# Optimization experiments

Measured on AMD Instinct MI355X. Metric: run time of the kernel, lower is better.

The kernel has to match this reference:

```python
import jax, jax.numpy as jnp
import numpy as np

T = 512        # num tokens
H = 2048       # hidden_size
I = 1024       # moe_intermediate_size
E = 32         # n_routed_experts
K = 8          # num_experts_per_tok
NG = 8         # n_group
TG = 4         # topk_group
NSH = 2        # n_shared_experts
SCALE = 2.5    # routed_scaling_factor


def setup_inputs() -> dict:
    key = jax.random.key(0)
    ks = jax.random.split(key, 7)
    s = 0.02  # weight init scale
    return {
        "hidden_states": jax.random.normal(ks[0], (T, H), jnp.float32),
        "gate_w": jax.random.normal(ks[1], (E, H), jnp.float32) * s,
        "gate_bias": jax.random.normal(ks[2], (E,), jnp.float32) * s,
        "w_gate_up": jax.random.normal(ks[3], (E, H, 2 * I), jnp.float32) * s,
        "w_down": jax.random.normal(ks[4], (E, I, H), jnp.float32) * s,
        "shared_w_gate_up": jax.random.normal(ks[5], (H, 2 * NSH * I), jnp.float32) * s,
        "shared_w_down": jax.random.normal(ks[6], (NSH * I, H), jnp.float32) * s,
    }


def _grouped_topk(logits, bias):
    # DeepSeek-V3 noaux_tc routing with sigmoid scoring.
    t = logits.shape[0]
    s = jax.nn.sigmoid(logits)                       # [T,E] routing weights source
    sc = s + bias[None, :]                           # scores used for selection only
    grp = sc.reshape(t, NG, E // NG)
    # group score = sum of top-2 expert scores in each group
    gscore = jax.lax.top_k(grp, 2)[0].sum(-1)        # [T,NG]
    _, gidx = jax.lax.top_k(gscore, TG)              # [T,TG]
    gmask = jnp.zeros((t, NG), bool).at[jnp.arange(t)[:, None], gidx].set(True)
    emask = jnp.repeat(gmask, E // NG, axis=1)       # [T,E]
    masked = jnp.where(emask, sc, -jnp.inf)
    _, ids = jax.lax.top_k(masked, K)                # [T,K] expert ids
    w = jnp.take_along_axis(s, ids, axis=1)          # weights from un-biased scores
    w = w / jnp.sum(w, -1, keepdims=True)            # renormalize
    return w * SCALE, ids


def reference(hidden_states, gate_w, gate_bias, w_gate_up, w_down,
              shared_w_gate_up, shared_w_down):
    x = hidden_states                                 # [T,H]
    logits = x @ gate_w.T                             # [T,E] (gate in fp32)
    w, ids = _grouped_topk(logits, gate_bias)
    t = x.shape[0]
    # scatter top-k weights into dense combine matrix [T,E]
    cw = jnp.zeros((t, E), x.dtype).at[jnp.arange(t)[:, None], ids].add(w)
    # routed experts: silu-gated MLP per expert, combined by routing weights
    gu = jnp.einsum('th,ehi->tei', x, w_gate_up)      # [T,E,2I]
    gate, up = jnp.split(gu, 2, axis=-1)
    act = jax.nn.silu(gate) * up                      # SiluAndMul, [T,E,I]
    act = act * cw[:, :, None]                        # apply combine weight pre-down
    routed = jnp.einsum('tei,eih->th', act, w_down)   # [T,H]
    # shared experts MLP
    sgu = x @ shared_w_gate_up
    sg, su = jnp.split(sgu, 2, axis=-1)
    shared = (jax.nn.silu(sg) * su) @ shared_w_down   # [T,H]
    return routed + shared
```

## Files before the change

### kernel.cpp

```cpp
#include <hip/hip_runtime.h>
#include <hip/hip_bf16.h>

#define T_TOK 512
#define HD    2048
#define ID    1024
#define NE    32
#define TOPK  8
#define NGRP  8
#define TGRP  4
#define NSH   2
#define SCALE 2.5f
#define NEXP  (NE + NSH)
#define KT1   64
#define KT2   32

typedef __attribute__((ext_vector_type(8))) short bf16x8;
typedef __attribute__((ext_vector_type(4))) float f32x4;
typedef unsigned short u16;
typedef unsigned long long u64;
typedef unsigned int u32;

__device__ __forceinline__ u16 f2bf(float f) {
    union { float f; u32 u; } a; a.f = f;
    u32 r = a.u + 0x7FFFu + ((a.u >> 16) & 1u);
    return (u16)(r >> 16);
}

__device__ __forceinline__ u32 pk2(float lo, float hi) {
    union { float f; u32 u; } a, b; a.f = lo; b.f = hi;
    u32 rl = a.u + 0x7FFFu + ((a.u >> 16) & 1u);
    u32 rh = b.u + 0x7FFFu + ((b.u >> 16) & 1u);
    return (rh & 0xFFFF0000u) | (rl >> 16);
}

__device__ __forceinline__ f32x4 mfma16(bf16x8 a, bf16x8 b, f32x4 c) {
    return __builtin_amdgcn_mfma_f32_16x16x32_bf16(a, b, c, 0, 0, 0);
}

union Q { uint4 q; bf16x8 v; };

__device__ __forceinline__ void glds16(const void* g, void* l) {
    __builtin_amdgcn_global_load_lds(
        (const __attribute__((address_space(1))) u32*)g,
        (__attribute__((address_space(3))) u32*)l, 16, 0, 0);
}

__device__ __forceinline__ bf16x8 bfrag(const float* Bt, int c, int g) {
    const int clo = c ^ (g << 4);
    const float* p_lo = Bt + g * 512 + clo;
    const float* p_hi = Bt + g * 512 + 2048 + (clo ^ 64);
    union { u32 d[4]; bf16x8 v; } r;
    r.d[0] = pk2(p_lo[0],   p_lo[128]);
    r.d[1] = pk2(p_lo[256], p_lo[384]);
    r.d[2] = pk2(p_hi[0],   p_hi[128]);
    r.d[3] = pk2(p_hi[256], p_hi[384]);
    return r.v;
}

__global__ __launch_bounds__(256) void k_xconv(const float* __restrict__ x,
                                               u16* __restrict__ xb) {
    int gt = blockIdx.x * 256 + threadIdx.x;
    const float* s = x + (size_t)(gt >> 6) * HD + (gt & 63) * 32;
    float v[32];
#pragma unroll
    for (int i = 0; i < 8; i++) {
        float4 f = *(const float4*)(s + i * 4);
        v[i*4] = f.x; v[i*4+1] = f.y; v[i*4+2] = f.z; v[i*4+3] = f.w;
    }
    union { u16 o[32]; uint4 q[4]; } pk;
#pragma unroll
    for (int g = 0; g < 4; g++)
#pragma unroll
        for (int jj = 0; jj < 8; jj++) {
            int r = (jj < 4) ? 4*g + jj : 4*g + 16 + (jj - 4);
            pk.o[g*8 + jj] = f2bf(v[r]);
        }
    uint4* d = (uint4*)(xb + (size_t)gt * 32);
#pragma unroll
    for (int i = 0; i < 4; i++) d[i] = pk.q[i];
}

__global__ __launch_bounds__(64) void k_route(const float* __restrict__ x,
                                              const float* __restrict__ gw,
                                              const float* __restrict__ gb,
                                              int* __restrict__ counts,
                                              int* __restrict__ tok_ids,
                                              float* __restrict__ tok_w,
                                              int* __restrict__ slotmap) {
    const int t = blockIdx.x, lane = threadIdx.x;
    __shared__ float xr[HD];
    __shared__ float slog[NE], ss[NE], scb[NE], smm[NE];
    for (int i = lane; i < HD; i += 64) xr[i] = x[(size_t)t * HD + i];
    __syncthreads();
    const int e = lane >> 1, half = lane & 1;
    const float4* w4 = (const float4*)(gw + (size_t)e * HD + half * 1024);
    const float4* x4 = (const float4*)(xr + half * 1024);
    float acc = 0.f;
#pragma unroll 8
    for (int i = 0; i < 256; i++) {
        float4 a = x4[i], b = w4[i];
        acc += a.x * b.x + a.y * b.y + a.z * b.z + a.w * b.w;
    }
    acc += __shfl_xor(acc, 1, 64);
    if (!half) slog[e] = acc;
    __syncthreads();
    if (lane == 0) {
        for (int i = 0; i < NE; i++) {
            float s = 1.f / (1.f + __expf(-slog[i]));
            ss[i] = s; scb[i] = s + gb[i];
        }
        float gsc[NGRP];
        for (int g = 0; g < NGRP; g++) {
            float a = scb[4*g], b = scb[4*g+1], c = scb[4*g+2], d = scb[4*g+3];
            float mab = fmaxf(a,b), nab = fminf(a,b), mcd = fmaxf(c,d), ncd = fminf(c,d);
            float m2 = (mab >= mcd) ? fmaxf(nab, mcd) : fmaxf(ncd, mab);
            gsc[g] = fmaxf(mab, mcd) + m2;
        }
        int gmask = 0;
        for (int it = 0; it < TGRP; it++) {
            float best = -1e30f; int bi = 0;
            for (int g = 0; g < NGRP; g++)
                if (!((gmask >> g) & 1) && gsc[g] > best) { best = gsc[g]; bi = g; }
            gmask |= 1 << bi;
        }
        for (int i = 0; i < NE; i++)
            smm[i] = ((gmask >> (i >> 2)) & 1) ? scb[i] : -1e30f;
        int ids[TOPK]; float wv[TOPK]; float wsum = 0.f;
        for (int k = 0; k < TOPK; k++) {
            float best = -1e31f; int bi = 0;
            for (int i = 0; i < NE; i++)
                if (smm[i] > best) { best = smm[i]; bi = i; }
            smm[bi] = -1e32f;
            ids[k] = bi; wv[k] = ss[bi]; wsum += ss[bi];
        }
        float inv = SCALE / wsum;
        for (int k = 0; k < TOPK; k++) {
            int ee = ids[k];
            int pos = atomicAdd(&counts[ee], 1);
            tok_ids[ee * T_TOK + pos] = t;
            tok_w[ee * T_TOK + pos] = wv[k] * inv;
            slotmap[t * TOPK + k] = (ee << 9) | pos;
        }
    }
}

__global__ void k_scan(const int* __restrict__ counts, int* __restrict__ offs) {
    if (threadIdx.x == 0) {
        int o = 0;
        for (int e = 0; e < NE; e++) { offs[e] = o; o += counts[e]; }
    }
}

__global__ __launch_bounds__(256, 3) void k_gemm1(
    const float* __restrict__ wgu, const float* __restrict__ wsgu,
    const u16* __restrict__ xb,
    const int* __restrict__ counts, const int* __restrict__ offs,
    const int* __restrict__ tok_ids, const float* __restrict__ tok_w,
    u16* __restrict__ act) {
    const int tid = threadIdx.x, lane = tid & 63, w = tid >> 6;
    const int nb = blockIdx.x, mt = blockIdx.y, e = blockIdx.z;
    int ne, base, NS, upo; const float* gp;
    if (e < NE) {
        ne = counts[e]; base = offs[e];
        gp = wgu + (size_t)e * (HD * 2 * ID) + nb * 64;
        NS = 2 * ID; upo = ID;
    } else {
        int s = e - NE; ne = T_TOK; base = T_TOK * TOPK + s * T_TOK;
        gp = wsgu + s * ID + nb * 64;
        NS = 2 * NSH * ID; upo = NSH * ID;
    }
    if (mt * 128 >= ne) return;

    __shared__ __align__(16) u16   Al[2][4096];
    __shared__ __align__(16) float Bl[2][4096];

    const int c0 = 2 * w, c1 = 2 * w + 1;
    int sl0 = mt*128 + c0*16 + (lane & 15); if (sl0 > ne-1) sl0 = ne-1;
    int sl1 = mt*128 + c1*16 + (lane & 15); if (sl1 > ne-1) sl1 = ne-1;
    const int t0 = (e < NE) ? tok_ids[e*T_TOK + sl0] : sl0;
    const int t1 = (e < NE) ? tok_ids[e*T_TOK + sl1] : sl1;
    const char* a0 = (const char*)xb + (u32)t0 * (HD*2) + (lane >> 4) * 16;
    const char* a1 = (const char*)xb + (u32)t1 * (HD*2) + (lane >> 4) * 16;

    const float* bsrc[4];
#pragma unroll
    for (int i = 0; i < 4; i++) {
        int kloc = 8*w + 2*i + (lane >> 5);
        int c4 = (4 * (lane & 31)) ^ (((kloc >> 2) & 7) << 4);
        const float* bp = (c4 < 64) ? (gp + c4) : (gp + upo + (c4 - 64));
        bsrc[i] = bp + (size_t)kloc * NS;
    }
    const size_t kstep = (size_t)32 * NS;

    auto stage = [&](int buf, int kt) {
        glds16(a0 + (u32)kt * 64, &Al[buf][c0 * 512]);
        glds16(a1 + (u32)kt * 64, &Al[buf][c1 * 512]);
#pragma unroll
        for (int i = 0; i < 4; i++)
            glds16(bsrc[i] + (size_t)kt * kstep, &Bl[buf][(8*w + 2*i) * 128]);
    };

    f32x4 accg[8], accu[8];
#pragma unroll
    for (int f = 0; f < 8; f++) {
        accg[f] = (f32x4){0.f,0.f,0.f,0.f};
        accu[f] = (f32x4){0.f,0.f,0.f,0.f};
    }

    const int cg = w * 16 + (lane & 15);
    const int g  = lane >> 4;

    stage(0, 0);
    int buf = 0;
    for (int kt = 0; kt < KT1; kt++) {
        if (kt + 1 < KT1) {
            stage(buf ^ 1, kt + 1);
            asm volatile("s_waitcnt vmcnt(6)" ::: "memory");
        } else {
            asm volatile("s_waitcnt vmcnt(0)" ::: "memory");
        }
        __builtin_amdgcn_s_barrier();
        Q qg, qu;
        qg.v = bfrag(Bl[buf], cg, g);
        qu.v = bfrag(Bl[buf], cg + 64, g);
#pragma unroll
        for (int f = 0; f < 8; f++) {
            Q qa;
            qa.q = *(const uint4*)&Al[buf][f * 512 + (lane >> 4) * 128 + (lane & 15) * 8];
            accg[f] = mfma16(qa.v, qg.v, accg[f]);
            accu[f] = mfma16(qa.v, qu.v, accu[f]);
        }
        __builtin_amdgcn_s_barrier();
        buf ^= 1;
    }

    const int icol = nb * 64 + w * 16 + (lane & 15);
    const int kt2 = icol >> 5, r = icol & 31;
    const int pos = kt2 * 32 + ((r & 16) ? (((r & 15) >> 2) * 8 + 4 + (r & 3))
                                         : ((r >> 2) * 8 + (r & 3)));
#pragma unroll
    for (int f = 0; f < 8; f++) {
#pragma unroll
        for (int j = 0; j < 4; j++) {
            int slot = mt * 128 + f * 16 + (lane >> 4) * 4 + j;
            if (slot < ne) {
                float cw = (e < NE) ? tok_w[e * T_TOK + slot] : 1.f;
                float gg = accg[f][j], uu = accu[f][j];
                float vv = gg / (1.f + __expf(-gg)) * uu * cw;
                act[(size_t)(base + slot) * ID + pos] = f2bf(vv);
            }
        }
    }
}

__global__ __launch_bounds__(256, 3) void k_gemm2(
    const float* __restrict__ wd, const float* __restrict__ wsd,
    const u16* __restrict__ act,
    const int* __restrict__ counts, const int* __restrict__ offs,
    float* __restrict__ part) {
    const int tid = threadIdx.x, lane = tid & 63, w = tid >> 6;
    const int nb = blockIdx.x, mt = blockIdx.y, e = blockIdx.z;
    int ne, base; const float* gp;
    if (e < NE) {
        ne = counts[e]; base = offs[e];
        gp = wd + (size_t)e * (ID * HD) + nb * 128;
    } else {
        int s = e - NE; ne = T_TOK; base = T_TOK * TOPK + s * T_TOK;
        gp = wsd + (size_t)s * (ID * HD) + nb * 128;
    }
    if (mt * 128 >= ne) return;
    const int NS = HD;

    __shared__ __align__(16) u16   Al[2][4096];
    __shared__ __align__(16) float Bl[2][4096];

    const int c0 = 2 * w, c1 = 2 * w + 1;
    int sl0 = mt*128 + c0*16 + (lane & 15); if (sl0 > ne-1) sl0 = ne-1;
    int sl1 = mt*128 + c1*16 + (lane & 15); if (sl1 > ne-1) sl1 = ne-1;
    const char* a0 = (const char*)act + (size_t)(base + sl0) * (ID*2) + (lane >> 4) * 16;
    const char* a1 = (const char*)act + (size_t)(base + sl1) * (ID*2) + (lane >> 4) * 16;

    const float* bsrc[4];
#pragma unroll
    for (int i = 0; i < 4; i++) {
        int kloc = 8*w + 2*i + (lane >> 5);
        int c4 = (4 * (lane & 31)) ^ (((kloc >> 2) & 7) << 4);
        bsrc[i] = gp + (size_t)kloc * NS + c4;
    }
    const size_t kstep = (size_t)32 * NS;

    auto stage = [&](int buf, int kt) {
        glds16(a0 + (u32)kt * 64, &Al[buf][c0 * 512]);
        glds16(a1 + (u32)kt * 64, &Al[buf][c1 * 512]);
#pragma unroll
        for (int i = 0; i < 4; i++)
            glds16(bsrc[i] + (size_t)kt * kstep, &Bl[buf][(8*w + 2*i) * 128]);
    };

    f32x4 acc[8][2];
#pragma unroll
    for (int f = 0; f < 8; f++) {
        acc[f][0] = (f32x4){0.f,0.f,0.f,0.f};
        acc[f][1] = (f32x4){0.f,0.f,0.f,0.f};
    }

    const int cA = w * 16 + (lane & 15);
    const int g  = lane >> 4;

    stage(0, 0);
    int buf = 0;
    for (int kt = 0; kt < KT2; kt++) {
        if (kt + 1 < KT2) {
            stage(buf ^ 1, kt + 1);
            asm volatile("s_waitcnt vmcnt(6)" ::: "memory");
        } else {
            asm volatile("s_waitcnt vmcnt(0)" ::: "memory");
        }
        __builtin_amdgcn_s_barrier();
        Q q0, q1;
        q0.v = bfrag(Bl[buf], cA, g);
        q1.v = bfrag(Bl[buf], cA + 64, g);
#pragma unroll
        for (int f = 0; f < 8; f++) {
            Q qa;
            qa.q = *(const uint4*)&Al[buf][f * 512 + (lane >> 4) * 128 + (lane & 15) * 8];
            acc[f][0] = mfma16(qa.v, q0.v, acc[f][0]);
            acc[f][1] = mfma16(qa.v, q1.v, acc[f][1]);
        }
        __builtin_amdgcn_s_barrier();
        buf ^= 1;
    }

    const int col0 = nb * 128 + w * 16 + (lane & 15);
#pragma unroll
    for (int f = 0; f < 8; f++) {
#pragma unroll
        for (int j = 0; j < 4; j++) {
            int slot = mt * 128 + f * 16 + (lane >> 4) * 4 + j;
            if (slot < ne) {
                float* pr = part + (size_t)(base + slot) * HD + col0;
                pr[0]  = acc[f][0][j];
                pr[64] = acc[f][1][j];
            }
        }
    }
}

__global__ __launch_bounds__(256) void k_combine(const float* __restrict__ part,
                                                 const int* __restrict__ offs,
                                                 const int* __restrict__ slotmap,
                                                 float* __restrict__ out) {
    const int t = blockIdx.x, tid = threadIdx.x;
    __shared__ int rows[16];
    if (tid < TOPK) {
        int pk = slotmap[t * TOPK + tid];
        rows[tid] = offs[pk >> 9] + (pk & 511);
    } else if (tid < TOPK + NSH) {
        rows[tid] = T_TOK * TOPK + (tid - TOPK) * T_TOK + t;
    }
    __syncthreads();
    float4 s0 = {0,0,0,0}, s1 = {0,0,0,0};
#pragma unroll
    for (int k = 0; k < TOPK + NSH; k++) {
        const float* p = part + (size_t)rows[k] * HD + tid * 8;
        float4 a = ((const float4*)p)[0], b = ((const float4*)p)[1];
        s0.x += a.x; s0.y += a.y; s0.z += a.z; s0.w += a.w;
        s1.x += b.x; s1.y += b.y; s1.z += b.z; s1.w += b.w;
    }
    float* o = out + (size_t)t * HD + tid * 8;
    ((float4*)o)[0] = s0;
    ((float4*)o)[1] = s1;
}

extern "C" void kernel_launch(void* const* d_in, const int* in_sizes, int n_in,
                              void* d_out, int out_size, void* d_ws, size_t ws_size,
                              hipStream_t stream) {
    const float* x    = (const float*)d_in[0];
    const float* gw   = (const float*)d_in[1];
    const float* gb   = (const float*)d_in[2];
    const float* wgu  = (const float*)d_in[3];
    const float* wd   = (const float*)d_in[4];
    const float* wsgu = (const float*)d_in[5];
    const float* wsd  = (const float*)d_in[6];
    float* out = (float*)d_out;

    char* wsb = (char*)d_ws;
    int*   counts  = (int*)(wsb);
    int*   offs    = (int*)(wsb + 128);
    int*   tok_ids = (int*)(wsb + 256);
    float* tok_w   = (float*)(wsb + 65792);
    int*   slotmap = (int*)(wsb + 131328);
    u16*   xb      = (u16*)(wsb + 147712);
    u16*   act     = (u16*)(wsb + 2244864);
    float* part    = (float*)(wsb + 12730624);

    hipMemsetAsync(counts, 0, 128, stream);
    k_xconv<<<dim3((T_TOK * 64) / 256), 256, 0, stream>>>(x, xb);
    k_route<<<dim3(T_TOK), 64, 0, stream>>>(x, gw, gb, counts, tok_ids, tok_w, slotmap);
    k_scan<<<dim3(1), 64, 0, stream>>>(counts, offs);
    k_gemm1<<<dim3(ID / 64, 4, NEXP), 256, 0, stream>>>(
        wgu, wsgu, xb, counts, offs, tok_ids, tok_w, act);
    k_gemm2<<<dim3(HD / 128, 4, NEXP), 256, 0, stream>>>(
        wd, wsd, act, counts, offs, part);
    k_combine<<<dim3(T_TOK), 256, 0, stream>>>(part, offs, slotmap, out);
}
```

Baseline: 413.6 us.

## Load A fragments directly from global and triple-buffer B tiles in LDS

Both expert GEMM kernels stop staging the A operand (token activations) through LDS. Each wave now reads its A fragments straight from global memory using precomputed per-fragment offsets. The freed LDS is used to triple-buffer the fp32 B weight tiles, with a prefetch distance of two and adjusted vmcnt waits. The risk is that every wave re-reads the same A rows, which raises global/L2 traffic. Also, the synchronous A loads consumed in the same iteration may force the compiler to drain outstanding B prefetches, exposing memory latency each k-step.

```diff
diff --git a/kernel.cpp b/kernel.cpp
--- a/kernel.cpp
+++ b/kernel.cpp
@@ -171,16 +171,17 @@
     }
     if (mt * 128 >= ne) return;
 
-    __shared__ __align__(16) u16   Al[2][4096];
-    __shared__ __align__(16) float Bl[2][4096];
-
-    const int c0 = 2 * w, c1 = 2 * w + 1;
-    int sl0 = mt*128 + c0*16 + (lane & 15); if (sl0 > ne-1) sl0 = ne-1;
-    int sl1 = mt*128 + c1*16 + (lane & 15); if (sl1 > ne-1) sl1 = ne-1;
-    const int t0 = (e < NE) ? tok_ids[e*T_TOK + sl0] : sl0;
-    const int t1 = (e < NE) ? tok_ids[e*T_TOK + sl1] : sl1;
-    const char* a0 = (const char*)xb + (u32)t0 * (HD*2) + (lane >> 4) * 16;
-    const char* a1 = (const char*)xb + (u32)t1 * (HD*2) + (lane >> 4) * 16;
+    __shared__ __align__(16) float Bl[3][4096];
+
+    const char* xbp = (const char*)xb;
+    u32 aoff[8];
+#pragma unroll
+    for (int f = 0; f < 8; f++) {
+        int sl = mt*128 + f*16 + (lane & 15);
+        if (sl > ne-1) sl = ne-1;
+        int tk = (e < NE) ? tok_ids[e*T_TOK + sl] : sl;
+        aoff[f] = (u32)tk * (HD*2) + (lane >> 4) * 16;
+    }
 
     const float* bsrc[4];
 #pragma unroll
@@ -193,8 +194,6 @@
     const size_t kstep = (size_t)32 * NS;
 
     auto stage = [&](int buf, int kt) {
-        glds16(a0 + (u32)kt * 64, &Al[buf][c0 * 512]);
-        glds16(a1 + (u32)kt * 64, &Al[buf][c1 * 512]);
 #pragma unroll
         for (int i = 0; i < 4; i++)
             glds16(bsrc[i] + (size_t)kt * kstep, &Bl[buf][(8*w + 2*i) * 128]);
@@ -211,11 +210,14 @@
     const int g  = lane >> 4;
 
     stage(0, 0);
-    int buf = 0;
+    stage(1, 1);
     for (int kt = 0; kt < KT1; kt++) {
-        if (kt + 1 < KT1) {
-            stage(buf ^ 1, kt + 1);
-            asm volatile("s_waitcnt vmcnt(6)" ::: "memory");
+        const int buf = kt % 3;
+        if (kt + 2 < KT1) {
+            stage((kt + 2) % 3, kt + 2);
+            asm volatile("s_waitcnt vmcnt(8)" ::: "memory");
+        } else if (kt + 1 < KT1) {
+            asm volatile("s_waitcnt vmcnt(4)" ::: "memory");
         } else {
             asm volatile("s_waitcnt vmcnt(0)" ::: "memory");
         }
@@ -223,15 +225,15 @@
         Q qg, qu;
         qg.v = bfrag(Bl[buf], cg, g);
         qu.v = bfrag(Bl[buf], cg + 64, g);
+        const u32 ko = (u32)kt * 64;
 #pragma unroll
         for (int f = 0; f < 8; f++) {
             Q qa;
-            qa.q = *(const uint4*)&Al[buf][f * 512 + (lane >> 4) * 128 + (lane & 15) * 8];
+            qa.q = *(const uint4*)(xbp + aoff[f] + ko);
             accg[f] = mfma16(qa.v, qg.v, accg[f]);
             accu[f] = mfma16(qa.v, qu.v, accu[f]);
         }
         __builtin_amdgcn_s_barrier();
-        buf ^= 1;
     }
 
     const int icol = nb * 64 + w * 16 + (lane & 15);
@@ -271,14 +273,16 @@
     if (mt * 128 >= ne) return;
     const int NS = HD;
 
-    __shared__ __align__(16) u16   Al[2][4096];
-    __shared__ __align__(16) float Bl[2][4096];
-
-    const int c0 = 2 * w, c1 = 2 * w + 1;
-    int sl0 = mt*128 + c0*16 + (lane & 15); if (sl0 > ne-1) sl0 = ne-1;
-    int sl1 = mt*128 + c1*16 + (lane & 15); if (sl1 > ne-1) sl1 = ne-1;
-    const char* a0 = (const char*)act + (size_t)(base + sl0) * (ID*2) + (lane >> 4) * 16;
-    const char* a1 = (const char*)act + (size_t)(base + sl1) * (ID*2) + (lane >> 4) * 16;
+    __shared__ __align__(16) float Bl[3][4096];
+
+    const char* ap = (const char*)act;
+    u32 aoff[8];
+#pragma unroll
+    for (int f = 0; f < 8; f++) {
+        int sl = mt*128 + f*16 + (lane & 15);
+        if (sl > ne-1) sl = ne-1;
+        aoff[f] = (u32)(base + sl) * (ID*2) + (lane >> 4) * 16;
+    }
 
     const float* bsrc[4];
 #pragma unroll
@@ -290,8 +294,6 @@
     const size_t kstep = (size_t)32 * NS;
 
     auto stage = [&](int buf, int kt) {
-        glds16(a0 + (u32)kt * 64, &Al[buf][c0 * 512]);
-        glds16(a1 + (u32)kt * 64, &Al[buf][c1 * 512]);
 #pragma unroll
         for (int i = 0; i < 4; i++)
             glds16(bsrc[i] + (size_t)kt * kstep, &Bl[buf][(8*w + 2*i) * 128]);
@@ -308,11 +310,14 @@
     const int g  = lane >> 4;
 
     stage(0, 0);
-    int buf = 0;
+    stage(1, 1);
     for (int kt = 0; kt < KT2; kt++) {
-        if (kt + 1 < KT2) {
-            stage(buf ^ 1, kt + 1);
-            asm volatile("s_waitcnt vmcnt(6)" ::: "memory");
+        const int buf = kt % 3;
+        if (kt + 2 < KT2) {
+            stage((kt + 2) % 3, kt + 2);
+            asm volatile("s_waitcnt vmcnt(8)" ::: "memory");
+        } else if (kt + 1 < KT2) {
+            asm volatile("s_waitcnt vmcnt(4)" ::: "memory");
         } else {
             asm volatile("s_waitcnt vmcnt(0)" ::: "memory");
         }
@@ -320,15 +325,15 @@
         Q q0, q1;
         q0.v = bfrag(Bl[buf], cA, g);
         q1.v = bfrag(Bl[buf], cA + 64, g);
+        const u32 ko = (u32)kt * 64;
 #pragma unroll
         for (int f = 0; f < 8; f++) {
             Q qa;
-            qa.q = *(const uint4*)&Al[buf][f * 512 + (lane >> 4) * 128 + (lane & 15) * 8];
+            qa.q = *(const uint4*)(ap + aoff[f] + ko);
             acc[f][0] = mfma16(qa.v, q0.v, acc[f][0]);
             acc[f][1] = mfma16(qa.v, q1.v, acc[f][1]);
         }
         __builtin_amdgcn_s_barrier();
-        buf ^= 1;
     }
 
     const int col0 = nb * 128 + w * 16 + (lane & 15);
```

New measurement: 691.0 us. 1.67x slower.

## Unfuse SiLU epilogue from gemm1 into a separate elementwise kernel with contiguous weight tiles

Applied to the files above, without the earlier changes.

gemm1 now reads 128 contiguous columns of the gate/up weight (instead of paired gate and up halves) and writes raw bf16 gate/up results to a new intermediate buffer. A new k_silu kernel applies SiLU, the up multiply and the routing weight, writing act in the permuted layout that gemm2 expects. k_scan becomes k_finalize, which also builds a flat per-slot combine-weight array. The aim is more contiguous weight loads in gemm1, at the cost of an extra round trip through a gu buffer twice the size of act, plus one more kernel launch.

```diff
diff --git a/kernel.cpp b/kernel.cpp
--- a/kernel.cpp
+++ b/kernel.cpp
@@ -13,6 +13,7 @@
 #define NEXP  (NE + NSH)
 #define KT1   64
 #define KT2   32
+#define NSLOT (T_TOK * TOPK + NSH * T_TOK)
 
 typedef __attribute__((ext_vector_type(8))) short bf16x8;
 typedef __attribute__((ext_vector_type(4))) float f32x4;
@@ -24,6 +25,10 @@
     union { float f; u32 u; } a; a.f = f;
     u32 r = a.u + 0x7FFFu + ((a.u >> 16) & 1u);
     return (u16)(r >> 16);
+}
+
+__device__ __forceinline__ float bf2f(u16 h) {
+    union { u32 u; float f; } z; z.u = (u32)h << 16; return z.f;
 }
 
 __device__ __forceinline__ u32 pk2(float lo, float hi) {
@@ -144,30 +149,43 @@
     }
 }
 
-__global__ void k_scan(const int* __restrict__ counts, int* __restrict__ offs) {
+__global__ __launch_bounds__(256) void k_finalize(const int* __restrict__ counts,
+                                                  int* __restrict__ offs,
+                                                  const float* __restrict__ tok_w,
+                                                  float* __restrict__ cwflat) {
+    __shared__ int so[NE];
     if (threadIdx.x == 0) {
         int o = 0;
-        for (int e = 0; e < NE; e++) { offs[e] = o; o += counts[e]; }
-    }
+        for (int e = 0; e < NE; e++) { offs[e] = o; so[e] = o; o += counts[e]; }
+    }
+    __syncthreads();
+    for (int e = 0; e < NE; e++) {
+        int ne = counts[e], b = so[e];
+        for (int i = threadIdx.x; i < ne; i += 256)
+            cwflat[b + i] = tok_w[e * T_TOK + i];
+    }
+    for (int i = T_TOK * TOPK + threadIdx.x; i < NSLOT; i += 256)
+        cwflat[i] = 1.f;
 }
 
 __global__ __launch_bounds__(256, 3) void k_gemm1(
     const float* __restrict__ wgu, const float* __restrict__ wsgu,
     const u16* __restrict__ xb,
     const int* __restrict__ counts, const int* __restrict__ offs,
-    const int* __restrict__ tok_ids, const float* __restrict__ tok_w,
-    u16* __restrict__ act) {
+    const int* __restrict__ tok_ids,
+    u16* __restrict__ gu) {
     const int tid = threadIdx.x, lane = tid & 63, w = tid >> 6;
     const int nb = blockIdx.x, mt = blockIdx.y, e = blockIdx.z;
-    int ne, base, NS, upo; const float* gp;
+    int ne, base, NS; const float* gp;
+    const int cb = nb * 128;
     if (e < NE) {
         ne = counts[e]; base = offs[e];
-        gp = wgu + (size_t)e * (HD * 2 * ID) + nb * 64;
-        NS = 2 * ID; upo = ID;
+        gp = wgu + (size_t)e * (HD * 2 * ID) + cb;
+        NS = 2 * ID;
     } else {
         int s = e - NE; ne = T_TOK; base = T_TOK * TOPK + s * T_TOK;
-        gp = wsgu + s * ID + nb * 64;
-        NS = 2 * NSH * ID; upo = NSH * ID;
+        gp = wsgu + ((cb < ID) ? (s * ID + cb) : (NSH * ID + s * ID + (cb - ID)));
+        NS = 2 * NSH * ID;
     }
     if (mt * 128 >= ne) return;
 
@@ -187,8 +205,7 @@
     for (int i = 0; i < 4; i++) {
         int kloc = 8*w + 2*i + (lane >> 5);
         int c4 = (4 * (lane & 31)) ^ (((kloc >> 2) & 7) << 4);
-        const float* bp = (c4 < 64) ? (gp + c4) : (gp + upo + (c4 - 64));
-        bsrc[i] = bp + (size_t)kloc * NS;
+        bsrc[i] = gp + (size_t)kloc * NS + c4;
     }
     const size_t kstep = (size_t)32 * NS;
 
@@ -200,14 +217,14 @@
             glds16(bsrc[i] + (size_t)kt * kstep, &Bl[buf][(8*w + 2*i) * 128]);
     };
 
-    f32x4 accg[8], accu[8];
+    f32x4 acc[8][2];
 #pragma unroll
     for (int f = 0; f < 8; f++) {
-        accg[f] = (f32x4){0.f,0.f,0.f,0.f};
-        accu[f] = (f32x4){0.f,0.f,0.f,0.f};
-    }
-
-    const int cg = w * 16 + (lane & 15);
+        acc[f][0] = (f32x4){0.f,0.f,0.f,0.f};
+        acc[f][1] = (f32x4){0.f,0.f,0.f,0.f};
+    }
+
+    const int cA = w * 16 + (lane & 15);
     const int g  = lane >> 4;
 
     stage(0, 0);
@@ -220,37 +237,54 @@
             asm volatile("s_waitcnt vmcnt(0)" ::: "memory");
         }
         __builtin_amdgcn_s_barrier();
-        Q qg, qu;
-        qg.v = bfrag(Bl[buf], cg, g);
-        qu.v = bfrag(Bl[buf], cg + 64, g);
+        Q q0, q1;
+        q0.v = bfrag(Bl[buf], cA, g);
+        q1.v = bfrag(Bl[buf], cA + 64, g);
 #pragma unroll
         for (int f = 0; f < 8; f++) {
             Q qa;
             qa.q = *(const uint4*)&Al[buf][f * 512 + (lane >> 4) * 128 + (lane & 15) * 8];
-            accg[f] = mfma16(qa.v, qg.v, accg[f]);
-            accu[f] = mfma16(qa.v, qu.v, accu[f]);
+            acc[f][0] = mfma16(qa.v, q0.v, acc[f][0]);
+            acc[f][1] = mfma16(qa.v, q1.v, acc[f][1]);
         }
         __builtin_amdgcn_s_barrier();
         buf ^= 1;
     }
 
-    const int icol = nb * 64 + w * 16 + (lane & 15);
-    const int kt2 = icol >> 5, r = icol & 31;
-    const int pos = kt2 * 32 + ((r & 16) ? (((r & 15) >> 2) * 8 + 4 + (r & 3))
-                                         : ((r >> 2) * 8 + (r & 3)));
+    const int col0 = cb + w * 16 + (lane & 15);
 #pragma unroll
     for (int f = 0; f < 8; f++) {
 #pragma unroll
         for (int j = 0; j < 4; j++) {
             int slot = mt * 128 + f * 16 + (lane >> 4) * 4 + j;
             if (slot < ne) {
-                float cw = (e < NE) ? tok_w[e * T_TOK + slot] : 1.f;
-                float gg = accg[f][j], uu = accu[f][j];
-                float vv = gg / (1.f + __expf(-gg)) * uu * cw;
-                act[(size_t)(base + slot) * ID + pos] = f2bf(vv);
+                u16* pr = gu + (size_t)(base + slot) * (2 * ID) + col0;
+                pr[0]  = f2bf(acc[f][0][j]);
+                pr[64] = f2bf(acc[f][1][j]);
             }
         }
     }
+}
+
+__global__ __launch_bounds__(256) void k_silu(const u16* __restrict__ gu,
+                                              const float* __restrict__ cwflat,
+                                              u16* __restrict__ act) {
+    const int s = blockIdx.x, t = threadIdx.x;
+    const float cw = cwflat[s];
+    const int c0 = t * 4;
+    const int kt2 = c0 >> 5, r0 = c0 & 31;
+    const int pb = kt2 * 32 + ((r0 & 16) ? (((r0 & 15) >> 2) * 8 + 4) : ((r0 >> 2) * 8));
+    const u16* gr = gu + (size_t)s * (2 * ID);
+    union { u16 u[4]; u64 h; } g4, u4, o4;
+    g4.h = *(const u64*)(gr + c0);
+    u4.h = *(const u64*)(gr + ID + c0);
+#pragma unroll
+    for (int j = 0; j < 4; j++) {
+        float gg = bf2f(g4.u[j]), uu = bf2f(u4.u[j]);
+        float v = gg / (1.f + __expf(-gg)) * uu * cw;
+        o4.u[j] = f2bf(v);
+    }
+    *(u64*)(act + (size_t)s * ID + pb) = o4.h;
 }
 
 __global__ __launch_bounds__(256, 3) void k_gemm2(
@@ -390,16 +424,19 @@
     int*   tok_ids = (int*)(wsb + 256);
     float* tok_w   = (float*)(wsb + 65792);
     int*   slotmap = (int*)(wsb + 131328);
-    u16*   xb      = (u16*)(wsb + 147712);
-    u16*   act     = (u16*)(wsb + 2244864);
-    float* part    = (float*)(wsb + 12730624);
+    float* cwflat  = (float*)(wsb + 147712);
+    u16*   xb      = (u16*)(wsb + 168192);
+    u16*   act     = (u16*)(wsb + 2265344);
+    u16*   gu      = (u16*)(wsb + 12751104);
+    float* part    = (float*)(wsb + 33722624);
 
     hipMemsetAsync(counts, 0, 128, stream);
     k_xconv<<<dim3((T_TOK * 64) / 256), 256, 0, stream>>>(x, xb);
     k_route<<<dim3(T_TOK), 64, 0, stream>>>(x, gw, gb, counts, tok_ids, tok_w, slotmap);
-    k_scan<<<dim3(1), 64, 0, stream>>>(counts, offs);
-    k_gemm1<<<dim3(ID / 64, 4, NEXP), 256, 0, stream>>>(
-        wgu, wsgu, xb, counts, offs, tok_ids, tok_w, act);
+    k_finalize<<<dim3(1), 256, 0, stream>>>(counts, offs, tok_w, cwflat);
+    k_gemm1<<<dim3(16, 4, NEXP), 256, 0, stream>>>(
+        wgu, wsgu, xb, counts, offs, tok_ids, gu);
+    k_silu<<<dim3(NSLOT), 256, 0, stream>>>(gu, cwflat, act);
     k_gemm2<<<dim3(HD / 128, 4, NEXP), 256, 0, stream>>>(
         wd, wsd, act, counts, offs, part);
     k_combine<<<dim3(T_TOK), 256, 0, stream>>>(part, offs, slotmap, out);
```

After: 425.5 us. +2.9%, slower.
